# Kernel tuning notes

Measured on AMD Instinct MI355X. Metric: run time of the kernel, lower is better.

Reference implementation:

```python
import jax, jax.numpy as jnp
import numpy as np

B, D, T = 4, 1024, 512      # z: [B, input_dim, T]
V, CD = 32000, 4096          # codebook: [codebook_size, codebook_dim]
EPS = 1e-12                  # F.normalize default eps


def setup_inputs() -> dict:
    key = jax.random.key(0)
    k1, k2, k3, k4 = jax.random.split(key, 4)
    z = jax.random.normal(k1, (B, D, T), dtype=jnp.float32)
    codebook = jax.random.normal(k2, (V, CD), dtype=jnp.float32) * 0.02
    cb_w = jax.random.normal(k3, (D, CD), dtype=jnp.float32) * 0.02  # torch Linear weight [out,in]
    cb_b = jax.random.normal(k4, (D,), dtype=jnp.float32) * 0.02
    return {"z": z, "codebook": codebook, "cb_w": cb_w, "cb_b": cb_b}


def _l2norm(x):
    n = jnp.sqrt(jnp.sum(x * x, axis=1, keepdims=True))
    return x / jnp.maximum(n, EPS)


def reference(z, codebook, cb_w, cb_b):
    # stride == 1, use_cblinear == True -> z_e = z
    z_e = z                                              # [B, D, T]
    proj_cb = codebook @ cb_w.T + cb_b                    # [V, D] cb_proj(codebook)

    # decode_latents
    enc = jnp.transpose(z_e, (0, 2, 1)).reshape(-1, D)    # (B*T, D)
    enc_n = _l2norm(enc)
    cb_n = _l2norm(proj_cb)
    dist = (jnp.sum(enc_n * enc_n, axis=1, keepdims=True)
            - 2.0 * enc_n @ cb_n.T
            + jnp.sum(cb_n * cb_n, axis=1)[None, :])      # (B*T, V)
    indices = jnp.argmax(-dist, axis=1).reshape(B, T)     # argmin distance
    z_q = jnp.transpose(proj_cb[indices], (0, 2, 1))      # gather un-normalized codes -> [B, D, T]

    commitment_loss = jnp.mean((z_e - jax.lax.stop_gradient(z_q)) ** 2, axis=(1, 2))  # [B]
    codebook_loss = jnp.mean((z_q - jax.lax.stop_gradient(z_e)) ** 2, axis=(1, 2))    # [B]
    z_q_st = z_e + jax.lax.stop_gradient(z_q - z_e)       # straight-through
    return z_q_st, indices, commitment_loss, codebook_loss
```

## Files before the change

kernel.cpp:

```cpp
#include <hip/hip_runtime.h>
#include <hip/hip_bf16.h>
#include <math.h>

#define B_  4
#define D_  1024
#define T_  512
#define V_  32000
#define CD_ 4096
#define NR  (B_*T_)
#define VT  (V_/128)

typedef __attribute__((ext_vector_type(8))) short short8v;
typedef __attribute__((ext_vector_type(4))) float f32x4;

#define MFMA16(a,b,c) __builtin_amdgcn_mfma_f32_16x16x32_bf16((a),(b),(c),0,0,0)

__device__ __forceinline__ unsigned short f2bf(float f) {
    return __builtin_bit_cast(unsigned short, __float2bfloat16(f));
}
__device__ __forceinline__ float bf2f(unsigned short u) {
    unsigned int v = ((unsigned int)u) << 16;
    return __builtin_bit_cast(float, v);
}
__device__ __forceinline__ void glds16(const unsigned short* g, unsigned short* l) {
    __builtin_amdgcn_global_load_lds(
        (const __attribute__((address_space(1))) unsigned int*)g,
        (__attribute__((address_space(3))) unsigned int*)l, 16, 0, 0);
}
__device__ __forceinline__ void cvt8(const float4& x, const float4& y,
                                     short8v& h, short8v& l) {
    float xs[8] = {x.x, x.y, x.z, x.w, y.x, y.y, y.z, y.w};
    #pragma unroll
    for (int e = 0; e < 8; ++e) {
        unsigned short hb = f2bf(xs[e]);
        h[e] = (short)hb;
        l[e] = (short)f2bf(xs[e] - bf2f(hb));
    }
}


__global__ __launch_bounds__(256) void vq_cvt(const float* __restrict__ x,
                                              unsigned short* __restrict__ hi,
                                              unsigned short* __restrict__ lo,
                                              size_t n4) {
    size_t stride = (size_t)gridDim.x * 256;
    for (size_t i = blockIdx.x * 256 + threadIdx.x; i < n4; i += stride) {
        float4 v = *(const float4*)(x + 4 * i);
        float xs[4] = {v.x, v.y, v.z, v.w};
        ushort4 h, l;
        unsigned short* hp = (unsigned short*)&h;
        unsigned short* lp = (unsigned short*)&l;
        #pragma unroll
        for (int e = 0; e < 4; ++e) {
            hp[e] = f2bf(xs[e]);
            lp[e] = f2bf(xs[e] - bf2f(hp[e]));
        }
        *(ushort4*)(hi + 4 * i) = h;
        *(ushort4*)(lo + 4 * i) = l;
    }
}

__global__ __launch_bounds__(256) void vq_gemm1_mfma(
    const float* __restrict__ A,
    const unsigned short* __restrict__ Bhi, const unsigned short* __restrict__ Blo,
    const float* __restrict__ bias,
    unsigned short* __restrict__ Phi, unsigned short* __restrict__ Plo)
{
    __shared__ unsigned short smem[2][4][4096];
    const int tid = threadIdx.x;
    const int lane = tid & 63, w = tid >> 6;
    const int wr = w >> 1, wc = w & 1;
    const int m_tile = blockIdx.y * 128;
    const int n_tile = blockIdx.x * 128;
    const int row16 = lane & 15, kg = lane >> 4;
    const int s0 = 2 * w, s1 = s0 + 1;
    const int lane8 = lane * 8, wr4 = wr * 4, wc4 = wc * 4;

    const float*          Ap0 = A   + (size_t)(m_tile + s0*16 + row16) * CD_ + kg*8;
    const float*          Ap1 = A   + (size_t)(m_tile + s1*16 + row16) * CD_ + kg*8;
    const unsigned short* Bp0 = Bhi + (size_t)(n_tile + s0*16 + row16) * CD_ + kg*8;
    const unsigned short* Bp1 = Bhi + (size_t)(n_tile + s1*16 + row16) * CD_ + kg*8;
    const unsigned short* Lp0 = Blo + (size_t)(n_tile + s0*16 + row16) * CD_ + kg*8;
    const unsigned short* Lp1 = Blo + (size_t)(n_tile + s1*16 + row16) * CD_ + kg*8;

    f32x4 acc[4][4];
    #pragma unroll
    for (int i = 0; i < 4; ++i)
        #pragma unroll
        for (int j = 0; j < 4; ++j) acc[i][j] = (f32x4){0.f, 0.f, 0.f, 0.f};

    float4 aw[4], al_[4];

    aw[0] = *(const float4*)(Ap0);     aw[1] = *(const float4*)(Ap0 + 4);
    aw[2] = *(const float4*)(Ap1);     aw[3] = *(const float4*)(Ap1 + 4);
    glds16(Bp0, (unsigned short*)&smem[0][2][s0*512]);
    glds16(Bp1, (unsigned short*)&smem[0][2][s1*512]);
    glds16(Lp0, (unsigned short*)&smem[0][3][s0*512]);
    glds16(Lp1, (unsigned short*)&smem[0][3][s1*512]);
    {
        short8v h0, l0, h1, l1;
        cvt8(aw[0], aw[1], h0, l0);
        cvt8(aw[2], aw[3], h1, l1);
        *(short8v*)&smem[0][0][s0*512 + lane8] = h0;
        *(short8v*)&smem[0][1][s0*512 + lane8] = l0;
        *(short8v*)&smem[0][0][s1*512 + lane8] = h1;
        *(short8v*)&smem[0][1][s1*512 + lane8] = l1;
    }
    aw[0] = *(const float4*)(Ap0 + 32); aw[1] = *(const float4*)(Ap0 + 36);
    aw[2] = *(const float4*)(Ap1 + 32); aw[3] = *(const float4*)(Ap1 + 36);
    __syncthreads();

    int cur = 0;
    const int NT = CD_ / 32;
    for (int t = 0; t < NT; ++t) {
        if (t + 1 < NT) {
            const size_t ko = (size_t)(t + 1) * 32;
            glds16(Bp0 + ko, (unsigned short*)&smem[cur^1][2][s0*512]);
            glds16(Bp1 + ko, (unsigned short*)&smem[cur^1][2][s1*512]);
            glds16(Lp0 + ko, (unsigned short*)&smem[cur^1][3][s0*512]);
            glds16(Lp1 + ko, (unsigned short*)&smem[cur^1][3][s1*512]);
            short8v h0, l0, h1, l1;
            cvt8(aw[0], aw[1], h0, l0);
            cvt8(aw[2], aw[3], h1, l1);
            *(short8v*)&smem[cur^1][0][s0*512 + lane8] = h0;
            *(short8v*)&smem[cur^1][1][s0*512 + lane8] = l0;
            *(short8v*)&smem[cur^1][0][s1*512 + lane8] = h1;
            *(short8v*)&smem[cur^1][1][s1*512 + lane8] = l1;
        }
        if (t + 2 < NT) {
            const size_t ko2 = (size_t)(t + 2) * 32;
            al_[0] = *(const float4*)(Ap0 + ko2);  al_[1] = *(const float4*)(Ap0 + ko2 + 4);
            al_[2] = *(const float4*)(Ap1 + ko2);  al_[3] = *(const float4*)(Ap1 + ko2 + 4);
        }
        short8v ah[4], av[4], bh[4], bl[4];
        #pragma unroll
        for (int f = 0; f < 4; ++f) {
            ah[f] = *(const short8v*)&smem[cur][0][(wr4+f)*512 + lane8];
            av[f] = *(const short8v*)&smem[cur][1][(wr4+f)*512 + lane8];
            bh[f] = *(const short8v*)&smem[cur][2][(wc4+f)*512 + lane8];
            bl[f] = *(const short8v*)&smem[cur][3][(wc4+f)*512 + lane8];
        }
        #pragma unroll
        for (int mf = 0; mf < 4; ++mf)
            #pragma unroll
            for (int nf = 0; nf < 4; ++nf) {
                acc[mf][nf] = MFMA16(ah[mf], bh[nf], acc[mf][nf]);
                acc[mf][nf] = MFMA16(ah[mf], bl[nf], acc[mf][nf]);
                acc[mf][nf] = MFMA16(av[mf], bh[nf], acc[mf][nf]);
            }
        __syncthreads();
        #pragma unroll
        for (int q = 0; q < 4; ++q) aw[q] = al_[q];
        cur ^= 1;
    }

    #pragma unroll
    for (int nf = 0; nf < 4; ++nf) {
        const int col = n_tile + wc*64 + nf*16 + row16;
        const float bv = bias[col];
        #pragma unroll
        for (int mf = 0; mf < 4; ++mf) {
            const int rbase = m_tile + wr*64 + mf*16 + kg*4;
            #pragma unroll
            for (int r = 0; r < 4; ++r) {
                float vv = acc[mf][nf][r] + bv;
                unsigned short h = f2bf(vv);
                unsigned short l = f2bf(vv - bf2f(h));
                size_t o = (size_t)(rbase + r) * D_ + col;
                Phi[o] = h; Plo[o] = l;
            }
        }
    }
}

__global__ __launch_bounds__(256) void vq_norms_pl(const unsigned short* __restrict__ ph,
                                                   const unsigned short* __restrict__ pl,
                                                   float* __restrict__ ninv) {
    const int row  = blockIdx.x * 4 + (threadIdx.x >> 6);
    const int lane = threadIdx.x & 63;
    float s = 0.f;
    #pragma unroll
    for (int q = 0; q < 2; ++q) {
        size_t o = (size_t)row * D_ + q * 512 + lane * 8;
        short8v h = *(const short8v*)(ph + o);
        short8v l = *(const short8v*)(pl + o);
        #pragma unroll
        for (int e = 0; e < 8; ++e) {
            float x = bf2f((unsigned short)h[e]) + bf2f((unsigned short)l[e]);
            s += x * x;
        }
    }
    #pragma unroll
    for (int off = 32; off >= 1; off >>= 1) s += __shfl_down(s, off);
    if (lane == 0) ninv[row] = 1.0f / fmaxf(sqrtf(s), 1e-12f);
}

__global__ __launch_bounds__(256) void vq_transpose_cvt(const float* __restrict__ z,
                                                        unsigned short* __restrict__ ehi,
                                                        unsigned short* __restrict__ elo) {
    __shared__ float tile[64][65];
    const int b = blockIdx.z, t0 = blockIdx.x * 64, d0 = blockIdx.y * 64;
    const int lane = threadIdx.x & 63, sub = threadIdx.x >> 6;
    for (int dd = sub; dd < 64; dd += 4)
        tile[dd][lane] = z[((size_t)b * D_ + d0 + dd) * T_ + t0 + lane];
    __syncthreads();
    for (int tt = sub; tt < 64; tt += 4) {
        float v = tile[lane][tt];
        unsigned short h = f2bf(v);
        unsigned short l = f2bf(v - bf2f(h));
        size_t o = (size_t)(b * T_ + t0 + tt) * D_ + d0 + lane;
        ehi[o] = h; elo[o] = l;
    }
}

__global__ __launch_bounds__(256) void vq_gemm2_mfma(
    const unsigned short* __restrict__ Ehi, const unsigned short* __restrict__ Elo,
    const unsigned short* __restrict__ Phi, const unsigned short* __restrict__ Plo,
    const float* __restrict__ ninv,
    float* __restrict__ pmax, int* __restrict__ pidx)
{
    __shared__ unsigned short smem[2][4][4096];
    __shared__ float redv[2][128];
    __shared__ int   redi[2][128];
    const int tid = threadIdx.x;
    const int lane = tid & 63, w = tid >> 6;
    const int wr = w >> 1, wc = w & 1;
    const int m_tile = blockIdx.x * 128;
    const int n_tile = blockIdx.y * 128;
    const int row16 = lane & 15, kg = lane >> 4;
    const int s0 = 2 * w, s1 = s0 + 1;
    const int lane8 = lane * 8, wr4 = wr * 4, wc4 = wc * 4;

    const unsigned short* Ap0 = Ehi + (size_t)(m_tile + s0*16 + row16) * D_ + kg*8;
    const unsigned short* Ap1 = Ehi + (size_t)(m_tile + s1*16 + row16) * D_ + kg*8;
    const unsigned short* Cp0 = Elo + (size_t)(m_tile + s0*16 + row16) * D_ + kg*8;
    const unsigned short* Cp1 = Elo + (size_t)(m_tile + s1*16 + row16) * D_ + kg*8;
    const unsigned short* Bp0 = Phi + (size_t)(n_tile + s0*16 + row16) * D_ + kg*8;
    const unsigned short* Bp1 = Phi + (size_t)(n_tile + s1*16 + row16) * D_ + kg*8;
    const unsigned short* Lp0 = Plo + (size_t)(n_tile + s0*16 + row16) * D_ + kg*8;
    const unsigned short* Lp1 = Plo + (size_t)(n_tile + s1*16 + row16) * D_ + kg*8;

    f32x4 acc[4][4];
    #pragma unroll
    for (int i = 0; i < 4; ++i)
        #pragma unroll
        for (int j = 0; j < 4; ++j) acc[i][j] = (f32x4){0.f, 0.f, 0.f, 0.f};

#define STG2(bb, ko) do { \
    glds16(Ap0 + (ko), (unsigned short*)&smem[bb][0][s0*512]); \
    glds16(Ap1 + (ko), (unsigned short*)&smem[bb][0][s1*512]); \
    glds16(Cp0 + (ko), (unsigned short*)&smem[bb][1][s0*512]); \
    glds16(Cp1 + (ko), (unsigned short*)&smem[bb][1][s1*512]); \
    glds16(Bp0 + (ko), (unsigned short*)&smem[bb][2][s0*512]); \
    glds16(Bp1 + (ko), (unsigned short*)&smem[bb][2][s1*512]); \
    glds16(Lp0 + (ko), (unsigned short*)&smem[bb][3][s0*512]); \
    glds16(Lp1 + (ko), (unsigned short*)&smem[bb][3][s1*512]); \
} while (0)

    STG2(0, 0);
    __syncthreads();
    int cur = 0;
    const int NT = D_ / 32;
    for (int t = 0; t < NT; ++t) {
        if (t + 1 < NT) STG2(cur^1, (size_t)(t + 1) * 32);
        short8v ah[4], av[4], bh[4], bl[4];
        #pragma unroll
        for (int f = 0; f < 4; ++f) {
            ah[f] = *(const short8v*)&smem[cur][0][(wr4+f)*512 + lane8];
            av[f] = *(const short8v*)&smem[cur][1][(wr4+f)*512 + lane8];
            bh[f] = *(const short8v*)&smem[cur][2][(wc4+f)*512 + lane8];
            bl[f] = *(const short8v*)&smem[cur][3][(wc4+f)*512 + lane8];
        }
        #pragma unroll
        for (int mf = 0; mf < 4; ++mf)
            #pragma unroll
            for (int nf = 0; nf < 4; ++nf) {
                acc[mf][nf] = MFMA16(ah[mf], bh[nf], acc[mf][nf]);
                acc[mf][nf] = MFMA16(ah[mf], bl[nf], acc[mf][nf]);
                acc[mf][nf] = MFMA16(av[mf], bh[nf], acc[mf][nf]);
            }
        __syncthreads();
        cur ^= 1;
    }
#undef STG2

    float nv[4];
    #pragma unroll
    for (int nf = 0; nf < 4; ++nf) nv[nf] = ninv[n_tile + wc*64 + nf*16 + row16];
    #pragma unroll
    for (int mf = 0; mf < 4; ++mf) {
        #pragma unroll
        for (int r = 0; r < 4; ++r) {
            float best = -INFINITY; int bi = 0x7fffffff;
            #pragma unroll
            for (int nf = 0; nf < 4; ++nf) {
                float v = acc[mf][nf][r] * nv[nf];
                int ci = n_tile + wc*64 + nf*16 + row16;
                if (v > best || (v == best && ci < bi)) { best = v; bi = ci; }
            }
            #pragma unroll
            for (int m = 8; m >= 1; m >>= 1) {
                float ov = __shfl_xor(best, m, 16);
                int   oi = __shfl_xor(bi,   m, 16);
                if (ov > best || (ov == best && oi < bi)) { best = ov; bi = oi; }
            }
            if (row16 == 0) {
                int rl = wr*64 + mf*16 + kg*4 + r;
                redv[wc][rl] = best; redi[wc][rl] = bi;
            }
        }
    }
    __syncthreads();
    if (tid < 128) {
        float v0 = redv[0][tid], v1 = redv[1][tid];
        int   i0 = redi[0][tid], i1 = redi[1][tid];
        bool t1 = (v1 > v0) || (v1 == v0 && i1 < i0);
        size_t o = (size_t)(m_tile + tid) * VT + blockIdx.y;
        pmax[o] = t1 ? v1 : v0;
        pidx[o] = t1 ? i1 : i0;
    }
}

__global__ __launch_bounds__(256) void vq_gather_pl(const unsigned short* __restrict__ ph,
                                                    const unsigned short* __restrict__ pl,
                                                    const int* __restrict__ idxw,
                                                    const float* __restrict__ z,
                                                    float* __restrict__ out0,
                                                    float* __restrict__ lpart) {
    __shared__ float zq[64][65];
    __shared__ int idx_s[64];
    __shared__ float wsum[4];
    const int b = blockIdx.z, t0 = blockIdx.x * 64, d0 = blockIdx.y * 64;
    const int tid = threadIdx.x;
    const int lane = tid & 63, sub = tid >> 6;
    if (tid < 64) idx_s[tid] = idxw[b * T_ + t0 + tid];
    __syncthreads();
    for (int tt = sub; tt < 64; tt += 4) {
        size_t o = (size_t)idx_s[tt] * D_ + d0 + lane;
        zq[tt][lane] = bf2f(ph[o]) + bf2f(pl[o]);
    }
    __syncthreads();
    float lacc = 0.f;
    for (int dd = sub; dd < 64; dd += 4) {
        const size_t base = ((size_t)b * D_ + d0 + dd) * T_ + t0 + lane;
        float q = zq[lane][dd];
        float zv = z[base];
        out0[base] = q;
        float dv = zv - q;
        lacc += dv * dv;
    }
    #pragma unroll
    for (int off = 32; off >= 1; off >>= 1) lacc += __shfl_down(lacc, off);
    if (lane == 0) wsum[sub] = lacc;
    __syncthreads();
    if (tid == 0)
        lpart[(blockIdx.z * 16 + blockIdx.y) * 8 + blockIdx.x] =
            wsum[0] + wsum[1] + wsum[2] + wsum[3];
}

__global__ __launch_bounds__(256) void vq_argmerge(const float* __restrict__ pmax,
                                                   const int* __restrict__ pidx,
                                                   int* __restrict__ idxw,
                                                   float* __restrict__ outI) {
    const int i = blockIdx.x * 256 + threadIdx.x;
    if (i >= NR) return;
    float best = -INFINITY; int bi = 0;
    for (int c = 0; c < VT; c++) {
        float v = pmax[(size_t)i * VT + c];
        if (v > best) { best = v; bi = pidx[(size_t)i * VT + c]; }
    }
    idxw[i] = bi;
    outI[i] = (float)bi;
}

__global__ void vq_loss(const float* __restrict__ lpart, float* __restrict__ outL) {
    const int b = threadIdx.x;
    if (b >= B_) return;
    float s = 0.f;
    for (int q = 0; q < 128; q++) s += lpart[b * 128 + q];
    s /= (float)(D_ * T_);
    outL[b]      = s;
    outL[B_ + b] = s;
}

__global__ __launch_bounds__(256) void vq_gemm1(const float* __restrict__ A,
                                                const float* __restrict__ Bm,
                                                const float* __restrict__ bias,
                                                float* __restrict__ C) {
    __shared__ float As[32][128];
    __shared__ float Bs[32][128];
    const int tid = threadIdx.x;
    const int tx = tid & 15, ty = tid >> 4;
    const int n_tile = blockIdx.x * 128;
    const int m_tile = blockIdx.y * 128;
    float acc[8][8];
    #pragma unroll
    for (int i = 0; i < 8; i++)
        #pragma unroll
        for (int j = 0; j < 8; j++) acc[i][j] = 0.f;
    const int lr = tid >> 1;
    const int lk = (tid & 1) * 16;
    const float* Aptr = A  + (size_t)(m_tile + lr) * CD_ + lk;
    const float* Bptr = Bm + (size_t)(n_tile + lr) * CD_ + lk;
    for (int k0 = 0; k0 < CD_; k0 += 32) {
        float4 av[4], bv[4];
        #pragma unroll
        for (int q = 0; q < 4; q++) {
            av[q] = *(const float4*)(Aptr + k0 + q * 4);
            bv[q] = *(const float4*)(Bptr + k0 + q * 4);
        }
        __syncthreads();
        #pragma unroll
        for (int q = 0; q < 4; q++) {
            As[lk+q*4+0][lr] = av[q].x; As[lk+q*4+1][lr] = av[q].y;
            As[lk+q*4+2][lr] = av[q].z; As[lk+q*4+3][lr] = av[q].w;
            Bs[lk+q*4+0][lr] = bv[q].x; Bs[lk+q*4+1][lr] = bv[q].y;
            Bs[lk+q*4+2][lr] = bv[q].z; Bs[lk+q*4+3][lr] = bv[q].w;
        }
        __syncthreads();
        #pragma unroll
        for (int kk = 0; kk < 32; kk++) {
            float4 a0 = *(const float4*)&As[kk][ty*8];
            float4 a1 = *(const float4*)&As[kk][ty*8+4];
            float4 b0 = *(const float4*)&Bs[kk][tx*8];
            float4 b1 = *(const float4*)&Bs[kk][tx*8+4];
            float a[8] = {a0.x,a0.y,a0.z,a0.w,a1.x,a1.y,a1.z,a1.w};
            float b[8] = {b0.x,b0.y,b0.z,b0.w,b1.x,b1.y,b1.z,b1.w};
            #pragma unroll
            for (int i = 0; i < 8; i++)
                #pragma unroll
                for (int j = 0; j < 8; j++)
                    acc[i][j] = fmaf(a[i], b[j], acc[i][j]);
        }
    }
    const int m0 = m_tile + ty * 8, n0 = n_tile + tx * 8;
    float bv0[8];
    #pragma unroll
    for (int j = 0; j < 8; j++) bv0[j] = bias[n0 + j];
    #pragma unroll
    for (int i = 0; i < 8; i++) {
        float4 r0 = {acc[i][0]+bv0[0], acc[i][1]+bv0[1], acc[i][2]+bv0[2], acc[i][3]+bv0[3]};
        float4 r1 = {acc[i][4]+bv0[4], acc[i][5]+bv0[5], acc[i][6]+bv0[6], acc[i][7]+bv0[7]};
        *(float4*)(C + (size_t)(m0+i)*D_ + n0)     = r0;
        *(float4*)(C + (size_t)(m0+i)*D_ + n0 + 4) = r1;
    }
}

__global__ __launch_bounds__(256) void vq_norms(const float* __restrict__ P,
                                                float* __restrict__ ninv) {
    const int row  = blockIdx.x * 4 + (threadIdx.x >> 6);
    const int lane = threadIdx.x & 63;
    const float* p = P + (size_t)row * D_;
    float s = 0.f;
    #pragma unroll
    for (int q = 0; q < 4; q++) {
        float4 v = *(const float4*)(p + q * 256 + lane * 4);
        s += v.x*v.x + v.y*v.y + v.z*v.z + v.w*v.w;
    }
    #pragma unroll
    for (int off = 32; off >= 1; off >>= 1) s += __shfl_down(s, off);
    if (lane == 0) ninv[row] = 1.0f / fmaxf(sqrtf(s), 1e-12f);
}

__global__ __launch_bounds__(256) void vq_transpose(const float* __restrict__ z,
                                                    float* __restrict__ enc) {
    __shared__ float tile[64][65];
    const int b = blockIdx.z, t0 = blockIdx.x * 64, d0 = blockIdx.y * 64;
    const int lane = threadIdx.x & 63, sub = threadIdx.x >> 6;
    for (int dd = sub; dd < 64; dd += 4)
        tile[dd][lane] = z[((size_t)b * D_ + d0 + dd) * T_ + t0 + lane];
    __syncthreads();
    for (int tt = sub; tt < 64; tt += 4)
        enc[(size_t)(b * T_ + t0 + tt) * D_ + d0 + lane] = tile[lane][tt];
}

__global__ __launch_bounds__(256) void vq_gemm2(const float* __restrict__ E,
                                                const float* __restrict__ P,
                                                const float* __restrict__ ninv,
                                                float* __restrict__ pmax,
                                                int* __restrict__ pidx) {
    __shared__ float As[32][128];
    __shared__ float Bs[32][128];
    __shared__ float redv[128][17];
    __shared__ int   redi[128][17];
    const int tid = threadIdx.x;
    const int tx = tid & 15, ty = tid >> 4;
    const int m_tile = blockIdx.x * 128;
    const int n_tile = blockIdx.y * 128;
    float acc[8][8];
    #pragma unroll
    for (int i = 0; i < 8; i++)
        #pragma unroll
        for (int j = 0; j < 8; j++) acc[i][j] = 0.f;
    const int lr = tid >> 1;
    const int lk = (tid & 1) * 16;
    const float* Eptr = E + (size_t)(m_tile + lr) * D_ + lk;
    const float* Pptr = P + (size_t)(n_tile + lr) * D_ + lk;
    for (int k0 = 0; k0 < D_; k0 += 32) {
        float4 av[4], bv[4];
        #pragma unroll
        for (int q = 0; q < 4; q++) {
            av[q] = *(const float4*)(Eptr + k0 + q * 4);
            bv[q] = *(const float4*)(Pptr + k0 + q * 4);
        }
        __syncthreads();
        #pragma unroll
        for (int q = 0; q < 4; q++) {
            As[lk+q*4+0][lr] = av[q].x; As[lk+q*4+1][lr] = av[q].y;
            As[lk+q*4+2][lr] = av[q].z; As[lk+q*4+3][lr] = av[q].w;
            Bs[lk+q*4+0][lr] = bv[q].x; Bs[lk+q*4+1][lr] = bv[q].y;
            Bs[lk+q*4+2][lr] = bv[q].z; Bs[lk+q*4+3][lr] = bv[q].w;
        }
        __syncthreads();
        #pragma unroll
        for (int kk = 0; kk < 32; kk++) {
            float4 a0 = *(const float4*)&As[kk][ty*8];
            float4 a1 = *(const float4*)&As[kk][ty*8+4];
            float4 b0 = *(const float4*)&Bs[kk][tx*8];
            float4 b1 = *(const float4*)&Bs[kk][tx*8+4];
            float a[8] = {a0.x,a0.y,a0.z,a0.w,a1.x,a1.y,a1.z,a1.w};
            float b[8] = {b0.x,b0.y,b0.z,b0.w,b1.x,b1.y,b1.z,b1.w};
            #pragma unroll
            for (int i = 0; i < 8; i++)
                #pragma unroll
                for (int j = 0; j < 8; j++)
                    acc[i][j] = fmaf(a[i], b[j], acc[i][j]);
        }
    }
    const int n0 = n_tile + tx * 8;
    float nv[8];
    #pragma unroll
    for (int j = 0; j < 8; j++) nv[j] = ninv[n0 + j];
    #pragma unroll
    for (int i = 0; i < 8; i++) {
        const int rl = ty * 8 + i;
        float best = -INFINITY; int bi = 0;
        #pragma unroll
        for (int j = 0; j < 8; j++) {
            float v = acc[i][j] * nv[j];
            if (v > best) { best = v; bi = n0 + j; }
        }
        redv[rl][tx] = best; redi[rl][tx] = bi;
    }
    __syncthreads();
    if (tid < 128) {
        float best = -INFINITY; int bi = 0;
        #pragma unroll
        for (int c = 0; c < 16; c++) {
            float v = redv[tid][c];
            if (v > best) { best = v; bi = redi[tid][c]; }
        }
        pmax[(size_t)(m_tile + tid) * VT + blockIdx.y] = best;
        pidx[(size_t)(m_tile + tid) * VT + blockIdx.y] = bi;
    }
}

__global__ __launch_bounds__(256) void vq_gather(const float* __restrict__ proj,
                                                 const int* __restrict__ idxw,
                                                 const float* __restrict__ z,
                                                 float* __restrict__ out0,
                                                 float* __restrict__ lpart) {
    __shared__ float zq[64][65];
    __shared__ int idx_s[64];
    __shared__ float wsum[4];
    const int b = blockIdx.z, t0 = blockIdx.x * 64, d0 = blockIdx.y * 64;
    const int tid = threadIdx.x;
    const int lane = tid & 63, sub = tid >> 6;
    if (tid < 64) idx_s[tid] = idxw[b * T_ + t0 + tid];
    __syncthreads();
    for (int tt = sub; tt < 64; tt += 4)
        zq[tt][lane] = proj[(size_t)idx_s[tt] * D_ + d0 + lane];
    __syncthreads();
    float lacc = 0.f;
    for (int dd = sub; dd < 64; dd += 4) {
        const size_t base = ((size_t)b * D_ + d0 + dd) * T_ + t0 + lane;
        float q  = zq[lane][dd];
        float zv = z[base];
        out0[base] = q;
        float dv = zv - q;
        lacc += dv * dv;
    }
    #pragma unroll
    for (int off = 32; off >= 1; off >>= 1) lacc += __shfl_down(lacc, off);
    if (lane == 0) wsum[sub] = lacc;
    __syncthreads();
    if (tid == 0)
        lpart[(blockIdx.z * 16 + blockIdx.y) * 8 + blockIdx.x] =
            wsum[0] + wsum[1] + wsum[2] + wsum[3];
}

extern "C" void kernel_launch(void* const* d_in, const int* in_sizes, int n_in,
                              void* d_out, int out_size, void* d_ws, size_t ws_size,
                              hipStream_t stream) {
    const float* z        = (const float*)d_in[0];
    const float* codebook = (const float*)d_in[1];
    const float* cb_w     = (const float*)d_in[2];
    const float* cb_b     = (const float*)d_in[3];

    float* out0 = (float*)d_out;
    float* outI = out0 + (size_t)B_*D_*T_;
    float* outL = outI + NR;

    char* p = (char*)d_ws;
    auto alloc = [&](size_t bytes) { char* r = p; p += (bytes + 255) & ~(size_t)255; return r; };
    unsigned short* w_hi = (unsigned short*)alloc((size_t)D_ * CD_ * 2);
    unsigned short* w_lo = (unsigned short*)alloc((size_t)D_ * CD_ * 2);
    unsigned short* p_hi = (unsigned short*)alloc((size_t)V_ * D_ * 2);
    unsigned short* p_lo = (unsigned short*)alloc((size_t)V_ * D_ * 2);
    unsigned short* e_hi = (unsigned short*)alloc((size_t)NR * D_ * 2);
    unsigned short* e_lo = (unsigned short*)alloc((size_t)NR * D_ * 2);
    float* ninv  = (float*)alloc((size_t)V_ * 4);
    float* pmax  = (float*)alloc((size_t)NR * VT * 4);
    int*   pidx  = (int*)  alloc((size_t)NR * VT * 4);
    int*   idxw  = (int*)  alloc((size_t)NR * 4);
    float* lpart = (float*)alloc((size_t)2048 * 4);
    size_t need = (size_t)(p - (char*)d_ws);

    if (ws_size >= need) {
        vq_cvt<<<1024, 256, 0, stream>>>(cb_w, w_hi, w_lo, (size_t)D_ * CD_ / 4);
        vq_gemm1_mfma<<<dim3(D_/128, V_/128), 256, 0, stream>>>(codebook, w_hi, w_lo,
                                                                cb_b, p_hi, p_lo);
        vq_norms_pl<<<V_/4, 256, 0, stream>>>(p_hi, p_lo, ninv);
        vq_transpose_cvt<<<dim3(T_/64, D_/64, B_), 256, 0, stream>>>(z, e_hi, e_lo);
        vq_gemm2_mfma<<<dim3(NR/128, V_/128), 256, 0, stream>>>(e_hi, e_lo, p_hi, p_lo,
                                                                ninv, pmax, pidx);
        vq_argmerge<<<NR/256, 256, 0, stream>>>(pmax, pidx, idxw, outI);
        vq_gather_pl<<<dim3(T_/64, D_/64, B_), 256, 0, stream>>>(p_hi, p_lo, idxw, z,
                                                                 out0, lpart);
        vq_loss<<<1, 64, 0, stream>>>(lpart, outL);
    } else {
        float* proj  = (float*)d_ws;
        float* enc   = proj + (size_t)V_ * D_;
        float* ninv2 = enc  + (size_t)NR * D_;
        float* pmax2 = ninv2 + V_;
        int*   pidx2 = (int*)(pmax2 + (size_t)NR * VT);
        int*   idxw2 = pidx2 + (size_t)NR * VT;
        float* lpart2 = (float*)(idxw2 + NR);

        vq_gemm1<<<dim3(D_/128, V_/128), 256, 0, stream>>>(codebook, cb_w, cb_b, proj);
        vq_norms<<<V_/4, 256, 0, stream>>>(proj, ninv2);
        vq_transpose<<<dim3(T_/64, D_/64, B_), 256, 0, stream>>>(z, enc);
        vq_gemm2<<<dim3(NR/128, V_/128), 256, 0, stream>>>(enc, proj, ninv2, pmax2, pidx2);
        vq_argmerge<<<NR/256, 256, 0, stream>>>(pmax2, pidx2, idxw2, outI);
        vq_gather<<<dim3(T_/64, D_/64, B_), 256, 0, stream>>>(proj, idxw2, z, out0, lpart2);
        vq_loss<<<1, 64, 0, stream>>>(lpart2, outL);
    }
}
```

Before: 1.634 ms.

## Use 256x256 8-wave MFMA tiles with explicit waitcnt pipelining for both GEMMs

Replaces the 128x128 4-wave GEMM kernels with a shared 256x256 tile core run by 8 waves. It loads hi/lo bf16 planes through global_load_lds double buffering with explicit vmcnt waits, barriers and s_setprio around MFMA bursts. It also adds an XCD-aware workgroup swizzle and pre-converts the codebook to bf16 hi/lo so gemm1 uses the new core. The aim is more reuse per loaded tile and better latency hiding in the two large GEMMs. The cost is an extra full codebook conversion pass and a larger workspace, and the fp32 fallback path is removed.

New measurement: 1.559 ms. -4.6%, faster.

```diff
diff --git a/kernel.cpp b/kernel.cpp
--- a/kernel.cpp
+++ b/kernel.cpp
@@ -8,12 +8,19 @@
 #define V_  32000
 #define CD_ 4096
 #define NR  (B_*T_)
-#define VT  (V_/128)
+#define VT2 (V_/256)
 
 typedef __attribute__((ext_vector_type(8))) short short8v;
 typedef __attribute__((ext_vector_type(4))) float f32x4;
 
 #define MFMA16(a,b,c) __builtin_amdgcn_mfma_f32_16x16x32_bf16((a),(b),(c),0,0,0)
+
+#define ASM_VMCNT8() asm volatile("s_waitcnt vmcnt(8)" ::: "memory")
+#define ASM_VMCNT0() asm volatile("s_waitcnt vmcnt(0)" ::: "memory")
+#define ASM_LGKM0()  asm volatile("s_waitcnt lgkmcnt(0)" ::: "memory")
+#define BARRIER()    do { asm volatile("" ::: "memory");            \
+                          __builtin_amdgcn_s_barrier();             \
+                          __builtin_amdgcn_sched_barrier(0); } while (0)
 
 __device__ __forceinline__ unsigned short f2bf(float f) {
     return __builtin_bit_cast(unsigned short, __float2bfloat16(f));
@@ -37,14 +44,18 @@
         l[e] = (short)f2bf(xs[e] - bf2f(hb));
     }
 }
-
+__device__ __forceinline__ int xcd_swz(int wg, int nwg) {
+    int q = nwg >> 3, r = nwg & 7;
+    int x = wg & 7, o = wg >> 3;
+    return (x < r ? x * (q + 1) : r * (q + 1) + (x - r) * q) + o;
+}
 
 __global__ __launch_bounds__(256) void vq_cvt(const float* __restrict__ x,
                                               unsigned short* __restrict__ hi,
                                               unsigned short* __restrict__ lo,
                                               size_t n4) {
     size_t stride = (size_t)gridDim.x * 256;
-    for (size_t i = blockIdx.x * 256 + threadIdx.x; i < n4; i += stride) {
+    for (size_t i = (size_t)blockIdx.x * 256 + threadIdx.x; i < n4; i += stride) {
         float4 v = *(const float4*)(x + 4 * i);
         float xs[4] = {v.x, v.y, v.z, v.w};
         ushort4 h, l;
@@ -57,6 +68,181 @@
         }
         *(ushort4*)(hi + 4 * i) = h;
         *(ushort4*)(lo + 4 * i) = l;
+    }
+}
+
+#define GEMM_CORE_8P(KD)                                                      \
+    f32x4 acc[8][4];                                                          \
+    _Pragma("unroll")                                                         \
+    for (int i = 0; i < 8; ++i)                                               \
+        _Pragma("unroll")                                                     \
+        for (int j = 0; j < 4; ++j) acc[i][j] = (f32x4){0.f, 0.f, 0.f, 0.f};  \
+    const int lane = threadIdx.x & 63, w = threadIdx.x >> 6;                  \
+    const int wr = w >> 2, wc = w & 3;                                        \
+    const int r16 = lane & 15, kg = lane >> 4;                                \
+    const int lane8 = lane * 8, wr8 = wr * 8, wc4 = wc * 4;                   \
+    const int pw = w >> 1;                                                    \
+    const unsigned short* gplane = (pw == 0) ? Ahp : (pw == 1) ? Alp          \
+                                   : (pw == 2) ? Bhp : Blp;                   \
+    const int baseRow = (pw < 2 ? mt : nt) + (w & 1) * 128 + r16;             \
+    const unsigned short* gsrc = gplane + (size_t)baseRow * (KD) + kg * 8;    \
+    unsigned short* lb0 = &smem[0][pw][(w & 1) * 4096 + lane8];               \
+    unsigned short* lb1 = &smem[1][pw][(w & 1) * 4096 + lane8];               \
+                                                  \
+    _Pragma("unroll")                                                         \
+    for (int q = 0; q < 8; ++q)                                               \
+        glds16(gsrc + (size_t)q * 16 * (KD), lb0 + q * 512);                  \
+    ASM_VMCNT0();                                                             \
+    BARRIER();                                                                \
+    const int NT = (KD) / 32;                                                 \
+    for (int t = 0; t < NT; ++t) {                                            \
+        const int cur = t & 1;                                                \
+                      \
+        if (t + 1 < NT) {                                                     \
+            unsigned short* lb = cur ? lb0 : lb1;                             \
+            const size_t kof = (size_t)(t + 1) * 32;                          \
+            _Pragma("unroll")                                                 \
+            for (int q = 0; q < 8; ++q)                                       \
+                glds16(gsrc + kof + (size_t)q * 16 * (KD), lb + q * 512);     \
+            ASM_VMCNT8();                                                     \
+        } else {                                                              \
+            ASM_VMCNT0();                                                     \
+        }                                                                     \
+        BARRIER();                                                            \
+        short8v bh[4], bl[4];                                                 \
+        _Pragma("unroll")                                                     \
+        for (int nf = 0; nf < 4; ++nf) {                                      \
+            bh[nf] = *(const short8v*)&smem[cur][2][(wc4 + nf) * 512 + lane8];\
+            bl[nf] = *(const short8v*)&smem[cur][3][(wc4 + nf) * 512 + lane8];\
+        }                                                                     \
+        {                                                                     \
+            short8v a0h = *(const short8v*)&smem[cur][0][(wr8 + 0) * 512 + lane8]; \
+            short8v a0l = *(const short8v*)&smem[cur][1][(wr8 + 0) * 512 + lane8]; \
+            short8v a1h = *(const short8v*)&smem[cur][0][(wr8 + 1) * 512 + lane8]; \
+            short8v a1l = *(const short8v*)&smem[cur][1][(wr8 + 1) * 512 + lane8]; \
+            __builtin_amdgcn_s_setprio(1);                                    \
+            _Pragma("unroll")                                                 \
+            for (int nf = 0; nf < 4; ++nf) {                                  \
+                acc[0][nf] = MFMA16(a0h, bh[nf], acc[0][nf]);                 \
+                acc[0][nf] = MFMA16(a0h, bl[nf], acc[0][nf]);                 \
+                acc[0][nf] = MFMA16(a0l, bh[nf], acc[0][nf]);                 \
+                acc[1][nf] = MFMA16(a1h, bh[nf], acc[1][nf]);                 \
+                acc[1][nf] = MFMA16(a1h, bl[nf], acc[1][nf]);                 \
+                acc[1][nf] = MFMA16(a1l, bh[nf], acc[1][nf]);                 \
+            }                                                                 \
+            __builtin_amdgcn_s_setprio(0);                                    \
+        }                                                                     \
+        BARRIER();                                                            \
+                                                             \
+        _Pragma("unroll")                                                     \
+        for (int j = 1; j < 4; ++j) {                                         \
+            short8v a0h = *(const short8v*)&smem[cur][0][(wr8 + 2*j) * 512 + lane8];     \
+            short8v a0l = *(const short8v*)&smem[cur][1][(wr8 + 2*j) * 512 + lane8];     \
+            short8v a1h = *(const short8v*)&smem[cur][0][(wr8 + 2*j + 1) * 512 + lane8]; \
+            short8v a1l = *(const short8v*)&smem[cur][1][(wr8 + 2*j + 1) * 512 + lane8]; \
+            BARRIER();                                                        \
+            __builtin_amdgcn_s_setprio(1);                                    \
+            _Pragma("unroll")                                                 \
+            for (int nf = 0; nf < 4; ++nf) {                                  \
+                acc[2*j][nf]   = MFMA16(a0h, bh[nf], acc[2*j][nf]);           \
+                acc[2*j][nf]   = MFMA16(a0h, bl[nf], acc[2*j][nf]);           \
+                acc[2*j][nf]   = MFMA16(a0l, bh[nf], acc[2*j][nf]);           \
+                acc[2*j+1][nf] = MFMA16(a1h, bh[nf], acc[2*j+1][nf]);         \
+                acc[2*j+1][nf] = MFMA16(a1h, bl[nf], acc[2*j+1][nf]);         \
+                acc[2*j+1][nf] = MFMA16(a1l, bh[nf], acc[2*j+1][nf]);         \
+            }                                                                 \
+            __builtin_amdgcn_s_setprio(0);                                    \
+            if (j < 3) BARRIER();                                             \
+        }                                                                     \
+        ASM_LGKM0();                                                          \
+        BARRIER();                                                            \
+    }
+
+__global__ __launch_bounds__(512, 2) void vq_gemm1_8p(
+    const unsigned short* __restrict__ Ahp, const unsigned short* __restrict__ Alp,
+    const unsigned short* __restrict__ Bhp, const unsigned short* __restrict__ Blp,
+    const float* __restrict__ bias,
+    unsigned short* __restrict__ Phi, unsigned short* __restrict__ Plo)
+{
+    __shared__ unsigned short smem[2][4][8192];
+    const int wg = xcd_swz(blockIdx.x, (V_/256) * (D_/256));
+    const int mt = (wg >> 2) * 256;
+    const int nt = (wg & 3) * 256;
+
+    GEMM_CORE_8P(CD_)
+
+    #pragma unroll
+    for (int nf = 0; nf < 4; ++nf) {
+        const int col = nt + wc * 64 + nf * 16 + r16;
+        const float bv = bias[col];
+        #pragma unroll
+        for (int mf = 0; mf < 8; ++mf) {
+            const int rbase = mt + wr * 128 + mf * 16 + kg * 4;
+            #pragma unroll
+            for (int r = 0; r < 4; ++r) {
+                float vv = acc[mf][nf][r] + bv;
+                unsigned short h = f2bf(vv);
+                unsigned short l = f2bf(vv - bf2f(h));
+                size_t o = (size_t)(rbase + r) * D_ + col;
+                Phi[o] = h; Plo[o] = l;
+            }
+        }
+    }
+}
+
+__global__ __launch_bounds__(512, 2) void vq_gemm2_8p(
+    const unsigned short* __restrict__ Ahp, const unsigned short* __restrict__ Alp,
+    const unsigned short* __restrict__ Bhp, const unsigned short* __restrict__ Blp,
+    const float* __restrict__ ninv,
+    float* __restrict__ pmax, int* __restrict__ pidx)
+{
+    __shared__ unsigned short smem[2][4][8192];
+    const int wg = xcd_swz(blockIdx.x, (NR/256) * VT2);
+    const int nid = wg >> 3;
+    const int mt = (wg & 7) * 256;
+    const int nt = nid * 256;
+
+    GEMM_CORE_8P(D_)
+
+    float* redv = (float*)&smem[0][0][0];
+    int*   redi = (int*)&smem[0][0][2048];
+    float nv[4];
+    #pragma unroll
+    for (int nf = 0; nf < 4; ++nf) nv[nf] = ninv[nt + wc * 64 + nf * 16 + r16];
+    #pragma unroll
+    for (int mf = 0; mf < 8; ++mf) {
+        #pragma unroll
+        for (int r = 0; r < 4; ++r) {
+            float best = -INFINITY; int bi = 0x7fffffff;
+            #pragma unroll
+            for (int nf = 0; nf < 4; ++nf) {
+                float v = acc[mf][nf][r] * nv[nf];
+                int ci = nt + wc * 64 + nf * 16 + r16;
+                if (v > best || (v == best && ci < bi)) { best = v; bi = ci; }
+            }
+            #pragma unroll
+            for (int m = 8; m >= 1; m >>= 1) {
+                float ov = __shfl_xor(best, m, 16);
+                int   oi = __shfl_xor(bi,   m, 16);
+                if (ov > best || (ov == best && oi < bi)) { best = ov; bi = oi; }
+            }
+            if (r16 == 0) {
+                int rl = wr * 128 + mf * 16 + kg * 4 + r;
+                redv[rl * 4 + wc] = best; redi[rl * 4 + wc] = bi;
+            }
+        }
+    }
+    BARRIER();
+    if (threadIdx.x < 256) {
+        float best = -INFINITY; int bi = 0x7fffffff;
+        #pragma unroll
+        for (int c = 0; c < 4; ++c) {
+            float v = redv[threadIdx.x * 4 + c];
+            int   i = redi[threadIdx.x * 4 + c];
+            if (v > best || (v == best && i < bi)) { best = v; bi = i; }
+        }
+        size_t o = (size_t)(mt + threadIdx.x) * VT2 + nid;
+        pmax[o] = best; pidx[o] = bi;
     }
 }
 
@@ -90,7 +276,6 @@
         for (int j = 0; j < 4; ++j) acc[i][j] = (f32x4){0.f, 0.f, 0.f, 0.f};
 
     float4 aw[4], al_[4];
-
     aw[0] = *(const float4*)(Ap0);     aw[1] = *(const float4*)(Ap0 + 4);
     aw[2] = *(const float4*)(Ap1);     aw[3] = *(const float4*)(Ap1 + 4);
     glds16(Bp0, (unsigned short*)&smem[0][2][s0*512]);
@@ -213,112 +398,21 @@
     }
 }
 
-__global__ __launch_bounds__(256) void vq_gemm2_mfma(
-    const unsigned short* __restrict__ Ehi, const unsigned short* __restrict__ Elo,
-    const unsigned short* __restrict__ Phi, const unsigned short* __restrict__ Plo,
-    const float* __restrict__ ninv,
-    float* __restrict__ pmax, int* __restrict__ pidx)
-{
-    __shared__ unsigned short smem[2][4][4096];
-    __shared__ float redv[2][128];
-    __shared__ int   redi[2][128];
-    const int tid = threadIdx.x;
-    const int lane = tid & 63, w = tid >> 6;
-    const int wr = w >> 1, wc = w & 1;
-    const int m_tile = blockIdx.x * 128;
-    const int n_tile = blockIdx.y * 128;
-    const int row16 = lane & 15, kg = lane >> 4;
-    const int s0 = 2 * w, s1 = s0 + 1;
-    const int lane8 = lane * 8, wr4 = wr * 4, wc4 = wc * 4;
-
-    const unsigned short* Ap0 = Ehi + (size_t)(m_tile + s0*16 + row16) * D_ + kg*8;
-    const unsigned short* Ap1 = Ehi + (size_t)(m_tile + s1*16 + row16) * D_ + kg*8;
-    const unsigned short* Cp0 = Elo + (size_t)(m_tile + s0*16 + row16) * D_ + kg*8;
-    const unsigned short* Cp1 = Elo + (size_t)(m_tile + s1*16 + row16) * D_ + kg*8;
-    const unsigned short* Bp0 = Phi + (size_t)(n_tile + s0*16 + row16) * D_ + kg*8;
-    const unsigned short* Bp1 = Phi + (size_t)(n_tile + s1*16 + row16) * D_ + kg*8;
-    const unsigned short* Lp0 = Plo + (size_t)(n_tile + s0*16 + row16) * D_ + kg*8;
-    const unsigned short* Lp1 = Plo + (size_t)(n_tile + s1*16 + row16) * D_ + kg*8;
-
-    f32x4 acc[4][4];
-    #pragma unroll
-    for (int i = 0; i < 4; ++i)
-        #pragma unroll
-        for (int j = 0; j < 4; ++j) acc[i][j] = (f32x4){0.f, 0.f, 0.f, 0.f};
-
-#define STG2(bb, ko) do { \
-    glds16(Ap0 + (ko), (unsigned short*)&smem[bb][0][s0*512]); \
-    glds16(Ap1 + (ko), (unsigned short*)&smem[bb][0][s1*512]); \
-    glds16(Cp0 + (ko), (unsigned short*)&smem[bb][1][s0*512]); \
-    glds16(Cp1 + (ko), (unsigned short*)&smem[bb][1][s1*512]); \
-    glds16(Bp0 + (ko), (unsigned short*)&smem[bb][2][s0*512]); \
-    glds16(Bp1 + (ko), (unsigned short*)&smem[bb][2][s1*512]); \
-    glds16(Lp0 + (ko), (unsigned short*)&smem[bb][3][s0*512]); \
-    glds16(Lp1 + (ko), (unsigned short*)&smem[bb][3][s1*512]); \
-} while (0)
-
-    STG2(0, 0);
-    __syncthreads();
-    int cur = 0;
-    const int NT = D_ / 32;
-    for (int t = 0; t < NT; ++t) {
-        if (t + 1 < NT) STG2(cur^1, (size_t)(t + 1) * 32);
-        short8v ah[4], av[4], bh[4], bl[4];
-        #pragma unroll
-        for (int f = 0; f < 4; ++f) {
-            ah[f] = *(const short8v*)&smem[cur][0][(wr4+f)*512 + lane8];
-            av[f] = *(const short8v*)&smem[cur][1][(wr4+f)*512 + lane8];
-            bh[f] = *(const short8v*)&smem[cur][2][(wc4+f)*512 + lane8];
-            bl[f] = *(const short8v*)&smem[cur][3][(wc4+f)*512 + lane8];
-        }
-        #pragma unroll
-        for (int mf = 0; mf < 4; ++mf)
-            #pragma unroll
-            for (int nf = 0; nf < 4; ++nf) {
-                acc[mf][nf] = MFMA16(ah[mf], bh[nf], acc[mf][nf]);
-                acc[mf][nf] = MFMA16(ah[mf], bl[nf], acc[mf][nf]);
-                acc[mf][nf] = MFMA16(av[mf], bh[nf], acc[mf][nf]);
-            }
-        __syncthreads();
-        cur ^= 1;
-    }
-#undef STG2
-
-    float nv[4];
-    #pragma unroll
-    for (int nf = 0; nf < 4; ++nf) nv[nf] = ninv[n_tile + wc*64 + nf*16 + row16];
-    #pragma unroll
-    for (int mf = 0; mf < 4; ++mf) {
-        #pragma unroll
-        for (int r = 0; r < 4; ++r) {
-            float best = -INFINITY; int bi = 0x7fffffff;
-            #pragma unroll
-            for (int nf = 0; nf < 4; ++nf) {
-                float v = acc[mf][nf][r] * nv[nf];
-                int ci = n_tile + wc*64 + nf*16 + row16;
-                if (v > best || (v == best && ci < bi)) { best = v; bi = ci; }
-            }
-            #pragma unroll
-            for (int m = 8; m >= 1; m >>= 1) {
-                float ov = __shfl_xor(best, m, 16);
-                int   oi = __shfl_xor(bi,   m, 16);
-                if (ov > best || (ov == best && oi < bi)) { best = ov; bi = oi; }
-            }
-            if (row16 == 0) {
-                int rl = wr*64 + mf*16 + kg*4 + r;
-                redv[wc][rl] = best; redi[wc][rl] = bi;
-            }
-        }
-    }
-    __syncthreads();
-    if (tid < 128) {
-        float v0 = redv[0][tid], v1 = redv[1][tid];
-        int   i0 = redi[0][tid], i1 = redi[1][tid];
-        bool t1 = (v1 > v0) || (v1 == v0 && i1 < i0);
-        size_t o = (size_t)(m_tile + tid) * VT + blockIdx.y;
-        pmax[o] = t1 ? v1 : v0;
-        pidx[o] = t1 ? i1 : i0;
-    }
+__global__ __launch_bounds__(256) void vq_argmerge(const float* __restrict__ pmax,
+                                                   const int* __restrict__ pidx,
+                                                   int* __restrict__ idxw,
+                                                   float* __restrict__ outI,
+                                                   int vt) {
+    const int i = blockIdx.x * 256 + threadIdx.x;
+    if (i >= NR) return;
+    float best = -INFINITY; int bi = 0;
+    for (int c = 0; c < vt; c++) {
+        float v = pmax[(size_t)i * vt + c];
+        int   ii = pidx[(size_t)i * vt + c];
+        if (v > best || (v == best && ii < bi)) { best = v; bi = ii; }
+    }
+    idxw[i] = bi;
+    outI[i] = (float)bi;
 }
 
 __global__ __launch_bounds__(256) void vq_gather_pl(const unsigned short* __restrict__ ph,
@@ -358,21 +452,6 @@
             wsum[0] + wsum[1] + wsum[2] + wsum[3];
 }
 
-__global__ __launch_bounds__(256) void vq_argmerge(const float* __restrict__ pmax,
-                                                   const int* __restrict__ pidx,
-                                                   int* __restrict__ idxw,
-                                                   float* __restrict__ outI) {
-    const int i = blockIdx.x * 256 + threadIdx.x;
-    if (i >= NR) return;
-    float best = -INFINITY; int bi = 0;
-    for (int c = 0; c < VT; c++) {
-        float v = pmax[(size_t)i * VT + c];
-        if (v > best) { best = v; bi = pidx[(size_t)i * VT + c]; }
-    }
-    idxw[i] = bi;
-    outI[i] = (float)bi;
-}
-
 __global__ void vq_loss(const float* __restrict__ lpart, float* __restrict__ outL) {
     const int b = threadIdx.x;
     if (b >= B_) return;
@@ -381,212 +460,6 @@
     s /= (float)(D_ * T_);
     outL[b]      = s;
     outL[B_ + b] = s;
-}
-
-__global__ __launch_bounds__(256) void vq_gemm1(const float* __restrict__ A,
-                                                const float* __restrict__ Bm,
-                                                const float* __restrict__ bias,
-                                                float* __restrict__ C) {
-    __shared__ float As[32][128];
-    __shared__ float Bs[32][128];
-    const int tid = threadIdx.x;
-    const int tx = tid & 15, ty = tid >> 4;
-    const int n_tile = blockIdx.x * 128;
-    const int m_tile = blockIdx.y * 128;
-    float acc[8][8];
-    #pragma unroll
-    for (int i = 0; i < 8; i++)
-        #pragma unroll
-        for (int j = 0; j < 8; j++) acc[i][j] = 0.f;
-    const int lr = tid >> 1;
-    const int lk = (tid & 1) * 16;
-    const float* Aptr = A  + (size_t)(m_tile + lr) * CD_ + lk;
-    const float* Bptr = Bm + (size_t)(n_tile + lr) * CD_ + lk;
-    for (int k0 = 0; k0 < CD_; k0 += 32) {
-        float4 av[4], bv[4];
-        #pragma unroll
-        for (int q = 0; q < 4; q++) {
-            av[q] = *(const float4*)(Aptr + k0 + q * 4);
-            bv[q] = *(const float4*)(Bptr + k0 + q * 4);
-        }
-        __syncthreads();
-        #pragma unroll
-        for (int q = 0; q < 4; q++) {
-            As[lk+q*4+0][lr] = av[q].x; As[lk+q*4+1][lr] = av[q].y;
-            As[lk+q*4+2][lr] = av[q].z; As[lk+q*4+3][lr] = av[q].w;
-            Bs[lk+q*4+0][lr] = bv[q].x; Bs[lk+q*4+1][lr] = bv[q].y;
-            Bs[lk+q*4+2][lr] = bv[q].z; Bs[lk+q*4+3][lr] = bv[q].w;
-        }
-        __syncthreads();
-        #pragma unroll
-        for (int kk = 0; kk < 32; kk++) {
-            float4 a0 = *(const float4*)&As[kk][ty*8];
-            float4 a1 = *(const float4*)&As[kk][ty*8+4];
-            float4 b0 = *(const float4*)&Bs[kk][tx*8];
-            float4 b1 = *(const float4*)&Bs[kk][tx*8+4];
-            float a[8] = {a0.x,a0.y,a0.z,a0.w,a1.x,a1.y,a1.z,a1.w};
-            float b[8] = {b0.x,b0.y,b0.z,b0.w,b1.x,b1.y,b1.z,b1.w};
-            #pragma unroll
-            for (int i = 0; i < 8; i++)
-                #pragma unroll
-                for (int j = 0; j < 8; j++)
-                    acc[i][j] = fmaf(a[i], b[j], acc[i][j]);
-        }
-    }
-    const int m0 = m_tile + ty * 8, n0 = n_tile + tx * 8;
-    float bv0[8];
-    #pragma unroll
-    for (int j = 0; j < 8; j++) bv0[j] = bias[n0 + j];
-    #pragma unroll
-    for (int i = 0; i < 8; i++) {
-        float4 r0 = {acc[i][0]+bv0[0], acc[i][1]+bv0[1], acc[i][2]+bv0[2], acc[i][3]+bv0[3]};
-        float4 r1 = {acc[i][4]+bv0[4], acc[i][5]+bv0[5], acc[i][6]+bv0[6], acc[i][7]+bv0[7]};
-        *(float4*)(C + (size_t)(m0+i)*D_ + n0)     = r0;
-        *(float4*)(C + (size_t)(m0+i)*D_ + n0 + 4) = r1;
-    }
-}
-
-__global__ __launch_bounds__(256) void vq_norms(const float* __restrict__ P,
-                                                float* __restrict__ ninv) {
-    const int row  = blockIdx.x * 4 + (threadIdx.x >> 6);
-    const int lane = threadIdx.x & 63;
-    const float* p = P + (size_t)row * D_;
-    float s = 0.f;
-    #pragma unroll
-    for (int q = 0; q < 4; q++) {
-        float4 v = *(const float4*)(p + q * 256 + lane * 4);
-        s += v.x*v.x + v.y*v.y + v.z*v.z + v.w*v.w;
-    }
-    #pragma unroll
-    for (int off = 32; off >= 1; off >>= 1) s += __shfl_down(s, off);
-    if (lane == 0) ninv[row] = 1.0f / fmaxf(sqrtf(s), 1e-12f);
-}
-
-__global__ __launch_bounds__(256) void vq_transpose(const float* __restrict__ z,
-                                                    float* __restrict__ enc) {
-    __shared__ float tile[64][65];
-    const int b = blockIdx.z, t0 = blockIdx.x * 64, d0 = blockIdx.y * 64;
-    const int lane = threadIdx.x & 63, sub = threadIdx.x >> 6;
-    for (int dd = sub; dd < 64; dd += 4)
-        tile[dd][lane] = z[((size_t)b * D_ + d0 + dd) * T_ + t0 + lane];
-    __syncthreads();
-    for (int tt = sub; tt < 64; tt += 4)
-        enc[(size_t)(b * T_ + t0 + tt) * D_ + d0 + lane] = tile[lane][tt];
-}
-
-__global__ __launch_bounds__(256) void vq_gemm2(const float* __restrict__ E,
-                                                const float* __restrict__ P,
-                                                const float* __restrict__ ninv,
-                                                float* __restrict__ pmax,
-                                                int* __restrict__ pidx) {
-    __shared__ float As[32][128];
-    __shared__ float Bs[32][128];
-    __shared__ float redv[128][17];
-    __shared__ int   redi[128][17];
-    const int tid = threadIdx.x;
-    const int tx = tid & 15, ty = tid >> 4;
-    const int m_tile = blockIdx.x * 128;
-    const int n_tile = blockIdx.y * 128;
-    float acc[8][8];
-    #pragma unroll
-    for (int i = 0; i < 8; i++)
-        #pragma unroll
-        for (int j = 0; j < 8; j++) acc[i][j] = 0.f;
-    const int lr = tid >> 1;
-    const int lk = (tid & 1) * 16;
-    const float* Eptr = E + (size_t)(m_tile + lr) * D_ + lk;
-    const float* Pptr = P + (size_t)(n_tile + lr) * D_ + lk;
-    for (int k0 = 0; k0 < D_; k0 += 32) {
-        float4 av[4], bv[4];
-        #pragma unroll
-        for (int q = 0; q < 4; q++) {
-            av[q] = *(const float4*)(Eptr + k0 + q * 4);
-            bv[q] = *(const float4*)(Pptr + k0 + q * 4);
-        }
-        __syncthreads();
-        #pragma unroll
-        for (int q = 0; q < 4; q++) {
-            As[lk+q*4+0][lr] = av[q].x; As[lk+q*4+1][lr] = av[q].y;
-            As[lk+q*4+2][lr] = av[q].z; As[lk+q*4+3][lr] = av[q].w;
-            Bs[lk+q*4+0][lr] = bv[q].x; Bs[lk+q*4+1][lr] = bv[q].y;
-            Bs[lk+q*4+2][lr] = bv[q].z; Bs[lk+q*4+3][lr] = bv[q].w;
-        }
-        __syncthreads();
-        #pragma unroll
-        for (int kk = 0; kk < 32; kk++) {
-            float4 a0 = *(const float4*)&As[kk][ty*8];
-            float4 a1 = *(const float4*)&As[kk][ty*8+4];
-            float4 b0 = *(const float4*)&Bs[kk][tx*8];
-            float4 b1 = *(const float4*)&Bs[kk][tx*8+4];
-            float a[8] = {a0.x,a0.y,a0.z,a0.w,a1.x,a1.y,a1.z,a1.w};
-            float b[8] = {b0.x,b0.y,b0.z,b0.w,b1.x,b1.y,b1.z,b1.w};
-            #pragma unroll
-            for (int i = 0; i < 8; i++)
-                #pragma unroll
-                for (int j = 0; j < 8; j++)
-                    acc[i][j] = fmaf(a[i], b[j], acc[i][j]);
-        }
-    }
-    const int n0 = n_tile + tx * 8;
-    float nv[8];
-    #pragma unroll
-    for (int j = 0; j < 8; j++) nv[j] = ninv[n0 + j];
-    #pragma unroll
-    for (int i = 0; i < 8; i++) {
-        const int rl = ty * 8 + i;
-        float best = -INFINITY; int bi = 0;
-        #pragma unroll
-        for (int j = 0; j < 8; j++) {
-            float v = acc[i][j] * nv[j];
-            if (v > best) { best = v; bi = n0 + j; }
-        }
-        redv[rl][tx] = best; redi[rl][tx] = bi;
-    }
-    __syncthreads();
-    if (tid < 128) {
-        float best = -INFINITY; int bi = 0;
-        #pragma unroll
-        for (int c = 0; c < 16; c++) {
-            float v = redv[tid][c];
-            if (v > best) { best = v; bi = redi[tid][c]; }
-        }
-        pmax[(size_t)(m_tile + tid) * VT + blockIdx.y] = best;
-        pidx[(size_t)(m_tile + tid) * VT + blockIdx.y] = bi;
-    }
-}
-
-__global__ __launch_bounds__(256) void vq_gather(const float* __restrict__ proj,
-                                                 const int* __restrict__ idxw,
-                                                 const float* __restrict__ z,
-                                                 float* __restrict__ out0,
-                                                 float* __restrict__ lpart) {
-    __shared__ float zq[64][65];
-    __shared__ int idx_s[64];
-    __shared__ float wsum[4];
-    const int b = blockIdx.z, t0 = blockIdx.x * 64, d0 = blockIdx.y * 64;
-    const int tid = threadIdx.x;
-    const int lane = tid & 63, sub = tid >> 6;
-    if (tid < 64) idx_s[tid] = idxw[b * T_ + t0 + tid];
-    __syncthreads();
-    for (int tt = sub; tt < 64; tt += 4)
-        zq[tt][lane] = proj[(size_t)idx_s[tt] * D_ + d0 + lane];
-    __syncthreads();
-    float lacc = 0.f;
-    for (int dd = sub; dd < 64; dd += 4) {
-        const size_t base = ((size_t)b * D_ + d0 + dd) * T_ + t0 + lane;
-        float q  = zq[lane][dd];
-        float zv = z[base];
-        out0[base] = q;
-        float dv = zv - q;
-        lacc += dv * dv;
-    }
-    #pragma unroll
-    for (int off = 32; off >= 1; off >>= 1) lacc += __shfl_down(lacc, off);
-    if (lane == 0) wsum[sub] = lacc;
-    __syncthreads();
-    if (tid == 0)
-        lpart[(blockIdx.z * 16 + blockIdx.y) * 8 + blockIdx.x] =
-            wsum[0] + wsum[1] + wsum[2] + wsum[3];
 }
 
 extern "C" void kernel_launch(void* const* d_in, const int* in_sizes, int n_in,
@@ -610,39 +483,30 @@
     unsigned short* e_hi = (unsigned short*)alloc((size_t)NR * D_ * 2);
     unsigned short* e_lo = (unsigned short*)alloc((size_t)NR * D_ * 2);
     float* ninv  = (float*)alloc((size_t)V_ * 4);
-    float* pmax  = (float*)alloc((size_t)NR * VT * 4);
-    int*   pidx  = (int*)  alloc((size_t)NR * VT * 4);
+    float* pmax  = (float*)alloc((size_t)NR * VT2 * 4);
+    int*   pidx  = (int*)  alloc((size_t)NR * VT2 * 4);
     int*   idxw  = (int*)  alloc((size_t)NR * 4);
     float* lpart = (float*)alloc((size_t)2048 * 4);
-    size_t need = (size_t)(p - (char*)d_ws);
-
-    if (ws_size >= need) {
-        vq_cvt<<<1024, 256, 0, stream>>>(cb_w, w_hi, w_lo, (size_t)D_ * CD_ / 4);
+    unsigned short* c_hi = (unsigned short*)alloc((size_t)V_ * CD_ * 2);
+    unsigned short* c_lo = (unsigned short*)alloc((size_t)V_ * CD_ * 2);
+    size_t need_full = (size_t)(p - (char*)d_ws);
+
+    vq_cvt<<<1024, 256, 0, stream>>>(cb_w, w_hi, w_lo, (size_t)D_ * CD_ / 4);
+    vq_transpose_cvt<<<dim3(T_/64, D_/64, B_), 256, 0, stream>>>(z, e_hi, e_lo);
+
+    if (ws_size >= need_full) {
+        vq_cvt<<<4096, 256, 0, stream>>>(codebook, c_hi, c_lo, (size_t)V_ * CD_ / 4);
+        vq_gemm1_8p<<<(V_/256) * (D_/256), 512, 0, stream>>>(c_hi, c_lo, w_hi, w_lo,
+                                                             cb_b, p_hi, p_lo);
+    } else {
         vq_gemm1_mfma<<<dim3(D_/128, V_/128), 256, 0, stream>>>(codebook, w_hi, w_lo,
                                                                 cb_b, p_hi, p_lo);
-        vq_norms_pl<<<V_/4, 256, 0, stream>>>(p_hi, p_lo, ninv);
-        vq_transpose_cvt<<<dim3(T_/64, D_/64, B_), 256, 0, stream>>>(z, e_hi, e_lo);
-        vq_gemm2_mfma<<<dim3(NR/128, V_/128), 256, 0, stream>>>(e_hi, e_lo, p_hi, p_lo,
-                                                                ninv, pmax, pidx);
-        vq_argmerge<<<NR/256, 256, 0, stream>>>(pmax, pidx, idxw, outI);
-        vq_gather_pl<<<dim3(T_/64, D_/64, B_), 256, 0, stream>>>(p_hi, p_lo, idxw, z,
-                                                                 out0, lpart);
-        vq_loss<<<1, 64, 0, stream>>>(lpart, outL);
-    } else {
-        float* proj  = (float*)d_ws;
-        float* enc   = proj + (size_t)V_ * D_;
-        float* ninv2 = enc  + (size_t)NR * D_;
-        float* pmax2 = ninv2 + V_;
-        int*   pidx2 = (int*)(pmax2 + (size_t)NR * VT);
-        int*   idxw2 = pidx2 + (size_t)NR * VT;
-        float* lpart2 = (float*)(idxw2 + NR);
-
-        vq_gemm1<<<dim3(D_/128, V_/128), 256, 0, stream>>>(codebook, cb_w, cb_b, proj);
-        vq_norms<<<V_/4, 256, 0, stream>>>(proj, ninv2);
-        vq_transpose<<<dim3(T_/64, D_/64, B_), 256, 0, stream>>>(z, enc);
-        vq_gemm2<<<dim3(NR/128, V_/128), 256, 0, stream>>>(enc, proj, ninv2, pmax2, pidx2);
-        vq_argmerge<<<NR/256, 256, 0, stream>>>(pmax2, pidx2, idxw2, outI);
-        vq_gather<<<dim3(T_/64, D_/64, B_), 256, 0, stream>>>(proj, idxw2, z, out0, lpart2);
-        vq_loss<<<1, 64, 0, stream>>>(lpart2, outL);
-    }
-}
+    }
+    vq_norms_pl<<<V_/4, 256, 0, stream>>>(p_hi, p_lo, ninv);
+    vq_gemm2_8p<<<(NR/256) * VT2, 512, 0, stream>>>(e_hi, e_lo, p_hi, p_lo,
+                                                    ninv, pmax, pidx);
+    vq_argmerge<<<NR/256, 256, 0, stream>>>(pmax, pidx, idxw, outI, VT2);
+    vq_gather_pl<<<dim3(T_/64, D_/64, B_), 256, 0, stream>>>(p_hi, p_lo, idxw, z,
+                                                             out0, lpart);
+    vq_loss<<<1, 64, 0, stream>>>(lpart, outL);
+}
```
